# Optimization experiments

Hardware: AMD Instinct MI355X
Metric: run time of the kernel (lower is better)

The kernel has to match this reference:

```python
import jax, jax.numpy as jnp
import numpy as np

D_MODEL = 1024
N_HEADS = 16
D_HEAD = D_MODEL // N_HEADS


def setup_inputs() -> dict:
    key = jax.random.key(0)
    k1, k2, k3 = jax.random.split(key, 3)
    x = jax.random.normal(k1, (2, 2048, D_MODEL), dtype=jnp.float32)
    # torch Linear weights transposed to [in, out] for x @ W
    w_qkv = jax.random.normal(k2, (D_MODEL, 3 * D_MODEL), dtype=jnp.float32) * (D_MODEL ** -0.5)
    w_proj = jax.random.normal(k3, (D_MODEL, D_MODEL), dtype=jnp.float32) * (D_MODEL ** -0.5)
    return {"x": x, "w_qkv": w_qkv, "w_proj": w_proj}


def reference(x, w_qkv, w_proj):
    B, N, D = x.shape
    qkv = x @ w_qkv                              # [B, N, 3D]
    q, k, v = jnp.split(qkv, 3, axis=-1)         # each [B, N, D]

    def split_heads(t):
        return t.reshape(B, N, N_HEADS, D_HEAD).transpose(0, 2, 1, 3)  # [B, H, N, d]

    q, k, v = map(split_heads, (q, k, v))
    scale = 1.0 / jnp.sqrt(jnp.float32(D_HEAD))
    scores = jnp.einsum('bhnd,bhmd->bhnm', q, k) * scale   # [B, H, N, N]
    attn = jax.nn.softmax(scores, axis=-1)
    out = jnp.einsum('bhnm,bhmd->bhnd', attn, v)            # [B, H, N, d]
    out = out.transpose(0, 2, 1, 3).reshape(B, N, D)        # merge heads
    return out @ w_proj + x
```

## Files before the change

kernel.cpp:

```cpp
#include <hip/hip_runtime.h>
#include <hip/hip_bf16.h>
#include <cstdint>
#include <cstddef>

typedef __bf16 bf16;
typedef __attribute__((ext_vector_type(4))) float f32x4;
typedef __attribute__((ext_vector_type(8))) __bf16 bf16x8;
typedef __attribute__((ext_vector_type(4))) __bf16 bf16x4;

#define D_MODEL 1024
#define NHEADS  16
#define DHEAD   64
#define SEQ     2048
#define BATCH   2
#define MROWS   (BATCH*SEQ)
#define BHTOT   (BATCH*NHEADS)

#define QSCALE 0.18033688011112042f
#define DEFER_THR 11.5f

__device__ __forceinline__ void gload16(const bf16* g, bf16* l) {
  __builtin_amdgcn_global_load_lds(
      (const __attribute__((address_space(1))) void*)g,
      (__attribute__((address_space(3))) void*)l, 16, 0, 0);
}

__device__ __forceinline__ f32x4 mfma16(bf16x8 a, bf16x8 b, f32x4 c) {
  return __builtin_amdgcn_mfma_f32_16x16x32_bf16(a, b, c, 0, 0, 0);
}

__device__ __forceinline__ float fexp2(float x) {
#if __has_builtin(__builtin_amdgcn_exp2f)
  return __builtin_amdgcn_exp2f(x);
#else
  float r; asm("v_exp_f32 %0, %1" : "=v"(r) : "v"(x)); return r;
#endif
}


__global__ void cast_f32_bf16(const float* __restrict__ in, bf16* __restrict__ out, int n4) {
  int i = blockIdx.x * blockDim.x + threadIdx.x;
  if (i >= n4) return;
  float4 v = ((const float4*)in)[i];
  bf16x4 o;
  o[0] = (bf16)v.x; o[1] = (bf16)v.y; o[2] = (bf16)v.z; o[3] = (bf16)v.w;
  ((bf16x4*)out)[i] = o;
}

__global__ void tcast(const float* __restrict__ in, bf16* __restrict__ out, int R, int C) {
  __shared__ float t[32][33];
  int c0 = blockIdx.x * 32, r0 = blockIdx.y * 32;
  int tx = threadIdx.x, ty = threadIdx.y;
  #pragma unroll
  for (int i = 0; i < 4; i++)
    t[ty + i*8][tx] = in[(size_t)(r0 + ty + i*8) * C + c0 + tx];
  __syncthreads();
  #pragma unroll
  for (int i = 0; i < 4; i++)
    out[(size_t)(c0 + ty + i*8) * R + r0 + tx] = (bf16)t[tx][ty + i*8];
}

__global__ void transpose_v(const bf16* __restrict__ v, bf16* __restrict__ vt) {
  __shared__ bf16 t[32][33];
  int bh = blockIdx.z;
  int r0 = blockIdx.x * 32;
  int d0 = blockIdx.y * 32;
  int tx = threadIdx.x, ty = threadIdx.y;
  const bf16* src = v + (size_t)bh * SEQ * DHEAD;
  bf16*       dst = vt + (size_t)bh * DHEAD * SEQ;
  #pragma unroll
  for (int i = 0; i < 4; i++)
    t[ty + i*8][tx] = src[(size_t)(r0 + ty + i*8) * DHEAD + d0 + tx];
  __syncthreads();
  #pragma unroll
  for (int i = 0; i < 4; i++)
    dst[(size_t)(d0 + ty + i*8) * SEQ + r0 + tx] = t[tx][ty + i*8];
}


template <int EPI>
__global__ __launch_bounds__(256, 3) void gemm_bt(
    const bf16* __restrict__ A, const bf16* __restrict__ Bt, int K, int N,
    bf16* __restrict__ qb, bf16* __restrict__ kb, bf16* __restrict__ vb,
    const float* __restrict__ xres, float* __restrict__ outf) {
  __shared__ alignas(16) bf16 As[128 * 64];
  __shared__ alignas(16) bf16 Bs[128 * 64];
  const int tid = threadIdx.x;
  const int wave = tid >> 6, lane = tid & 63;
  const int wr = wave >> 1, wc = wave & 1;
  const int m0 = blockIdx.y * 128, n0 = blockIdx.x * 128;
  const int srow = lane >> 3;
  const int scol = ((lane & 7) ^ srow) * 8;
  const int lr16 = lane & 15, lg = lane >> 4;
  const int rsw = (lr16 & 7) << 4;
  const int cA = (lg * 16) ^ rsw;
  const int cB = (64 + lg * 16) ^ rsw;
  const char* aP = (const char*)As + (wr*64 + lr16) * 128;
  const char* bP = (const char*)Bs + (wc*64 + lr16) * 128;

  f32x4 acc[4][4];
  #pragma unroll
  for (int m = 0; m < 4; m++)
    #pragma unroll
    for (int n = 0; n < 4; n++) acc[m][n] = (f32x4)0.0f;

  for (int k0 = 0; k0 < K; k0 += 64) {
    #pragma unroll
    for (int j = 0; j < 4; j++) {
      const int c = wave * 4 + j;
      gload16(A  + (size_t)(m0 + c*8 + srow) * K + k0 + scol, &As[c * 512]);
      gload16(Bt + (size_t)(n0 + c*8 + srow) * K + k0 + scol, &Bs[c * 512]);
    }
    __syncthreads();
    bf16x8 af[4][2], bfr[4][2];
    #pragma unroll
    for (int m = 0; m < 4; m++) {
      af[m][0] = *(const bf16x8*)(aP + m*2048 + cA);
      af[m][1] = *(const bf16x8*)(aP + m*2048 + cB);
    }
    #pragma unroll
    for (int n = 0; n < 4; n++) {
      bfr[n][0] = *(const bf16x8*)(bP + n*2048 + cA);
      bfr[n][1] = *(const bf16x8*)(bP + n*2048 + cB);
    }
    #pragma unroll
    for (int m = 0; m < 4; m++)
      #pragma unroll
      for (int n = 0; n < 4; n++) {
        acc[m][n] = mfma16(af[m][0], bfr[n][0], acc[m][n]);
        acc[m][n] = mfma16(af[m][1], bfr[n][1], acc[m][n]);
      }
    __syncthreads();
  }

  #pragma unroll
  for (int n = 0; n < 4; n++) {
    const int colg = n0 + wc*64 + n*16 + lr16;
    if (EPI == 0) {
      const int which = colg >> 10;
      const int win = colg & 1023;
      const int h = win >> 6, d = win & 63;
      bf16* dst = (which == 0) ? qb : (which == 1) ? kb : vb;
      const float sc = (which == 0) ? QSCALE : 1.0f;
      #pragma unroll
      for (int m = 0; m < 4; m++) {
        const int rowg0 = m0 + wr*64 + m*16 + lg*4;
        #pragma unroll
        for (int j = 0; j < 4; j++) {
          const int rowg = rowg0 + j;
          const int b = rowg >> 11, r = rowg & 2047;
          dst[((size_t)((b << 4) + h) * SEQ + r) * DHEAD + d] = (bf16)(acc[m][n][j] * sc);
        }
      }
    } else {
      #pragma unroll
      for (int m = 0; m < 4; m++) {
        const int rowg0 = m0 + wr*64 + m*16 + lg*4;
        #pragma unroll
        for (int j = 0; j < 4; j++) {
          const size_t idx = (size_t)(rowg0 + j) * N + colg;
          outf[idx] = acc[m][n][j] + xres[idx];
        }
      }
    }
  }
}

__global__ __launch_bounds__(512, 4) void attn_kernel(
    const bf16* __restrict__ q, const bf16* __restrict__ k,
    const bf16* __restrict__ vt, bf16* __restrict__ o) {
  __shared__ alignas(16) bf16 Ks[2][64 * 64];
  __shared__ alignas(16) bf16 Vs[2][64 * 64];
  __shared__ alignas(16) bf16 P[8][16 * 72];
  const int tid = threadIdx.x;
  const int wave = tid >> 6, lane = tid & 63;
  const int lr16 = lane & 15, lg = lane >> 4;
  const int bh = blockIdx.y;
  const int b = bh >> 4, h = bh & 15;
  const int qr = blockIdx.x * 128 + wave * 16;
  const bf16* kh = k  + (size_t)bh * SEQ * DHEAD;
  const bf16* vh = vt + (size_t)bh * DHEAD * SEQ;

  const int srow = lane >> 3;
  const int scol = ((lane & 7) ^ srow) * 8;
  const bf16* kg = kh + (size_t)(wave*8 + srow) * DHEAD + scol;
  const bf16* vg = vh + (size_t)(wave*8 + srow) * SEQ + scol;
  bf16* ldsK0 = &Ks[0][wave * 512];
  bf16* ldsK1 = &Ks[1][wave * 512];
  bf16* ldsV0 = &Vs[0][wave * 512];
  bf16* ldsV1 = &Vs[1][wave * 512];

  const bf16* qrow = q + (size_t)bh * SEQ * DHEAD + (size_t)(qr + lr16) * DHEAD;
  bf16x8 qf[2];
  qf[0] = *(const bf16x8*)&qrow[lg * 8];
  qf[1] = *(const bf16x8*)&qrow[32 + lg * 8];

  float mr = 0.0f, lsum = 0.0f;
  f32x4 acc[4];
  #pragma unroll
  for (int db = 0; db < 4; db++) acc[db] = (f32x4)0.0f;

  const int rsw = (lr16 & 7) << 4;
  const int cA = (lg * 16) ^ rsw;
  const int cB = (64 + lg * 16) ^ rsw;
  const char* kr0 = (const char*)&Ks[0][0] + lr16 * 128;
  const char* kr1 = (const char*)&Ks[1][0] + lr16 * 128;
  const char* vr0 = (const char*)&Vs[0][0] + lr16 * 128;
  const char* vr1 = (const char*)&Vs[1][0] + lr16 * 128;
  bf16* pww = &P[wave][lr16 * 72 + lg * 4];
  const bf16* pfr = &P[wave][lr16 * 72 + lg * 8];

  auto compute = [&](const char* kr, const char* vr) {
    const float nmr = -mr;
    f32x4 s[4];
    __builtin_amdgcn_s_setprio(1);
    #pragma unroll
    for (int i = 0; i < 4; i++) {
      bf16x8 kf0 = *(const bf16x8*)(kr + i*2048 + cA);
      bf16x8 kf1 = *(const bf16x8*)(kr + i*2048 + cB);
      f32x4 z = {nmr, nmr, nmr, nmr};
      z = mfma16(kf0, qf[0], z);
      z = mfma16(kf1, qf[1], z);
      s[i] = z;
    }
    __builtin_amdgcn_s_setprio(0);

    float u0 = fmaxf(fmaxf(s[0][0], s[0][1]), s[0][2]);
    float u1 = fmaxf(fmaxf(s[0][3], s[1][0]), s[1][1]);
    float u2 = fmaxf(fmaxf(s[1][2], s[1][3]), s[2][0]);
    float u3 = fmaxf(fmaxf(s[2][1], s[2][2]), s[2][3]);
    float u4 = fmaxf(fmaxf(s[3][0], s[3][1]), s[3][2]);
    float lmax = fmaxf(fmaxf(fmaxf(u0, u1), fmaxf(u2, u3)), fmaxf(u4, s[3][3]));

    if (!__all(lmax <= DEFER_THR)) {
      float mx = fmaxf(lmax, __shfl_xor(lmax, 16));
      mx = fmaxf(mx, __shfl_xor(mx, 32));
      mx = fmaxf(mx, 0.0f);
      const float corr = fexp2(-mx);
      lsum *= corr;
      #pragma unroll
      for (int db = 0; db < 4; db++) acc[db] *= corr;
      mr += mx;
      #pragma unroll
      for (int i = 0; i < 4; i++)
        #pragma unroll
        for (int r = 0; r < 4; r++) s[i][r] -= mx;
    }

    #pragma unroll
    for (int i = 0; i < 4; i++)
      #pragma unroll
      for (int r = 0; r < 4; r++) s[i][r] = fexp2(s[i][r]);
    lsum += ((s[0][0] + s[0][1]) + (s[0][2] + s[0][3]))
          + ((s[1][0] + s[1][1]) + (s[1][2] + s[1][3]))
          + ((s[2][0] + s[2][1]) + (s[2][2] + s[2][3]))
          + ((s[3][0] + s[3][1]) + (s[3][2] + s[3][3]));

    #pragma unroll
    for (int i = 0; i < 4; i++) {
      bf16x4 pv;
      #pragma unroll
      for (int r = 0; r < 4; r++) pv[r] = (bf16)s[i][r];
      *(bf16x4*)(pww + i * 16) = pv;
    }
    bf16x8 pf0 = *(const bf16x8*)pfr;
    bf16x8 pf1 = *(const bf16x8*)(pfr + 32);

    __builtin_amdgcn_s_setprio(1);
    #pragma unroll
    for (int db = 0; db < 4; db++) {
      bf16x8 vf0 = *(const bf16x8*)(vr + db*2048 + cA);
      bf16x8 vf1 = *(const bf16x8*)(vr + db*2048 + cB);
      acc[db] = mfma16(vf0, pf0, acc[db]);
      acc[db] = mfma16(vf1, pf1, acc[db]);
    }
    __builtin_amdgcn_s_setprio(0);
  };

  gload16(kg, ldsK0); gload16(vg, ldsV0);
  kg += 64 * DHEAD; vg += 64;
  __syncthreads();

  for (int t = 0; t < SEQ / 64; t += 2) {
    gload16(kg, ldsK1); gload16(vg, ldsV1);
    kg += 64 * DHEAD; vg += 64;
    compute(kr0, vr0);
    __syncthreads();
    if (t + 2 < SEQ / 64) {
      gload16(kg, ldsK0); gload16(vg, ldsV0);
      kg += 64 * DHEAD; vg += 64;
    }
    compute(kr1, vr1);
    __syncthreads();
  }

  lsum += __shfl_xor(lsum, 16);
  lsum += __shfl_xor(lsum, 32);
  const float inv = 1.0f / lsum;
  bf16* orow = o + ((size_t)(b * SEQ + qr + lr16)) * D_MODEL + h * 64;
  #pragma unroll
  for (int db = 0; db < 4; db++) {
    bf16x4 ov;
    #pragma unroll
    for (int r = 0; r < 4; r++) ov[r] = (bf16)(acc[db][r] * inv);
    *(bf16x4*)&orow[db * 16 + lg * 4] = ov;
  }
}


extern "C" void kernel_launch(void* const* d_in, const int* in_sizes, int n_in,
                              void* d_out, int out_size, void* d_ws, size_t ws_size,
                              hipStream_t stream) {
  const float* x      = (const float*)d_in[0];
  const float* w_qkv  = (const float*)d_in[1];
  const float* w_proj = (const float*)d_in[2];
  float* outf = (float*)d_out;

  bf16* xb    = (bf16*)d_ws;
  bf16* wqkvT = xb    + (size_t)MROWS * D_MODEL;
  bf16* wpT   = wqkvT + (size_t)3 * D_MODEL * D_MODEL;
  bf16* qb    = wpT   + (size_t)D_MODEL * D_MODEL;
  bf16* kb    = qb    + (size_t)BHTOT * SEQ * DHEAD;
  bf16* vb    = kb    + (size_t)BHTOT * SEQ * DHEAD;
  bf16* vt    = xb;
  bf16* ob    = vb;

  dim3 tb(32, 8);

  cast_f32_bf16<<<(MROWS * D_MODEL / 4 + 255) / 256, 256, 0, stream>>>(
      x, xb, MROWS * D_MODEL / 4);
  tcast<<<dim3(3 * D_MODEL / 32, D_MODEL / 32), tb, 0, stream>>>(
      w_qkv, wqkvT, D_MODEL, 3 * D_MODEL);
  tcast<<<dim3(D_MODEL / 32, D_MODEL / 32), tb, 0, stream>>>(
      w_proj, wpT, D_MODEL, D_MODEL);

  gemm_bt<0><<<dim3(3 * D_MODEL / 128, MROWS / 128), 256, 0, stream>>>(
      xb, wqkvT, D_MODEL, 3 * D_MODEL, qb, kb, vb, nullptr, nullptr);

  transpose_v<<<dim3(SEQ / 32, DHEAD / 32, BHTOT), tb, 0, stream>>>(vb, vt);

  attn_kernel<<<dim3(SEQ / 128, BHTOT), 512, 0, stream>>>(qb, kb, vt, ob);

  gemm_bt<1><<<dim3(D_MODEL / 128, MROWS / 128), 256, 0, stream>>>(
      ob, wpT, D_MODEL, D_MODEL, nullptr, nullptr, nullptr, x, outf);
}
```

Measured before the change: 131.0 us.

## Switch attention to 32x32 MFMA with register-shuffled P and fuse V transpose

Rewrites the attention kernel so each wave handles 32 query rows using 32x32x16 bf16 MFMA. The probability tile is now built in registers with packed bf16 converts and cross-half lane shuffles instead of a round trip through shared memory. The QKV GEMM epilogue writes V already transposed, which removes the separate transpose kernel and its extra global traffic. In exchange, blocks drop to 256 threads, register pressure rises, and the transposed V stores from the GEMM are strided and less coalesced.

```diff
diff --git a/kernel.cpp b/kernel.cpp
--- a/kernel.cpp
+++ b/kernel.cpp
@@ -5,8 +5,10 @@
 
 typedef __bf16 bf16;
 typedef __attribute__((ext_vector_type(4))) float f32x4;
+typedef __attribute__((ext_vector_type(16))) float f32x16;
 typedef __attribute__((ext_vector_type(8))) __bf16 bf16x8;
 typedef __attribute__((ext_vector_type(4))) __bf16 bf16x4;
+typedef __attribute__((ext_vector_type(4))) unsigned int u32x4;
 
 #define D_MODEL 1024
 #define NHEADS  16
@@ -29,12 +31,22 @@
   return __builtin_amdgcn_mfma_f32_16x16x32_bf16(a, b, c, 0, 0, 0);
 }
 
+__device__ __forceinline__ f32x16 mfma32(bf16x8 a, bf16x8 b, f32x16 c) {
+  return __builtin_amdgcn_mfma_f32_32x32x16_bf16(a, b, c, 0, 0, 0);
+}
+
 __device__ __forceinline__ float fexp2(float x) {
 #if __has_builtin(__builtin_amdgcn_exp2f)
   return __builtin_amdgcn_exp2f(x);
 #else
   float r; asm("v_exp_f32 %0, %1" : "=v"(r) : "v"(x)); return r;
 #endif
+}
+
+__device__ __forceinline__ unsigned cvtpk(float lo, float hi) {
+  unsigned r;
+  asm("v_cvt_pk_bf16_f32 %0, %1, %2" : "=v"(r) : "v"(lo), "v"(hi));
+  return r;
 }
 
 
@@ -60,28 +72,11 @@
     out[(size_t)(c0 + ty + i*8) * R + r0 + tx] = (bf16)t[tx][ty + i*8];
 }
 
-__global__ void transpose_v(const bf16* __restrict__ v, bf16* __restrict__ vt) {
-  __shared__ bf16 t[32][33];
-  int bh = blockIdx.z;
-  int r0 = blockIdx.x * 32;
-  int d0 = blockIdx.y * 32;
-  int tx = threadIdx.x, ty = threadIdx.y;
-  const bf16* src = v + (size_t)bh * SEQ * DHEAD;
-  bf16*       dst = vt + (size_t)bh * DHEAD * SEQ;
-  #pragma unroll
-  for (int i = 0; i < 4; i++)
-    t[ty + i*8][tx] = src[(size_t)(r0 + ty + i*8) * DHEAD + d0 + tx];
-  __syncthreads();
-  #pragma unroll
-  for (int i = 0; i < 4; i++)
-    dst[(size_t)(d0 + ty + i*8) * SEQ + r0 + tx] = t[tx][ty + i*8];
-}
-
 
 template <int EPI>
 __global__ __launch_bounds__(256, 3) void gemm_bt(
     const bf16* __restrict__ A, const bf16* __restrict__ Bt, int K, int N,
-    bf16* __restrict__ qb, bf16* __restrict__ kb, bf16* __restrict__ vb,
+    bf16* __restrict__ qb, bf16* __restrict__ kb, bf16* __restrict__ vtb,
     const float* __restrict__ xres, float* __restrict__ outf) {
   __shared__ alignas(16) bf16 As[128 * 64];
   __shared__ alignas(16) bf16 Bs[128 * 64];
@@ -140,8 +135,6 @@
       const int which = colg >> 10;
       const int win = colg & 1023;
       const int h = win >> 6, d = win & 63;
-      bf16* dst = (which == 0) ? qb : (which == 1) ? kb : vb;
-      const float sc = (which == 0) ? QSCALE : 1.0f;
       #pragma unroll
       for (int m = 0; m < 4; m++) {
         const int rowg0 = m0 + wr*64 + m*16 + lg*4;
@@ -149,7 +142,14 @@
         for (int j = 0; j < 4; j++) {
           const int rowg = rowg0 + j;
           const int b = rowg >> 11, r = rowg & 2047;
-          dst[((size_t)((b << 4) + h) * SEQ + r) * DHEAD + d] = (bf16)(acc[m][n][j] * sc);
+          const int bh = (b << 4) + h;
+          if (which == 2) {
+            vtb[((size_t)bh * DHEAD + d) * SEQ + r] = (bf16)acc[m][n][j];
+          } else {
+            bf16* dst = (which == 0) ? qb : kb;
+            const float sc = (which == 0) ? QSCALE : 1.0f;
+            dst[((size_t)bh * SEQ + r) * DHEAD + d] = (bf16)(acc[m][n][j] * sc);
+          }
         }
       }
     } else {
@@ -166,144 +166,148 @@
   }
 }
 
-__global__ __launch_bounds__(512, 4) void attn_kernel(
+__global__ __launch_bounds__(256, 2) void attn_kernel(
     const bf16* __restrict__ q, const bf16* __restrict__ k,
     const bf16* __restrict__ vt, bf16* __restrict__ o) {
   __shared__ alignas(16) bf16 Ks[2][64 * 64];
   __shared__ alignas(16) bf16 Vs[2][64 * 64];
-  __shared__ alignas(16) bf16 P[8][16 * 72];
   const int tid = threadIdx.x;
   const int wave = tid >> 6, lane = tid & 63;
-  const int lr16 = lane & 15, lg = lane >> 4;
+  const int l31 = lane & 31, hi = lane >> 5;
   const int bh = blockIdx.y;
   const int b = bh >> 4, h = bh & 15;
-  const int qr = blockIdx.x * 128 + wave * 16;
+  const int qr = blockIdx.x * 128 + wave * 32;
   const bf16* kh = k  + (size_t)bh * SEQ * DHEAD;
   const bf16* vh = vt + (size_t)bh * DHEAD * SEQ;
 
   const int srow = lane >> 3;
   const int scol = ((lane & 7) ^ srow) * 8;
-  const bf16* kg = kh + (size_t)(wave*8 + srow) * DHEAD + scol;
-  const bf16* vg = vh + (size_t)(wave*8 + srow) * SEQ + scol;
-  bf16* ldsK0 = &Ks[0][wave * 512];
-  bf16* ldsK1 = &Ks[1][wave * 512];
-  bf16* ldsV0 = &Vs[0][wave * 512];
-  bf16* ldsV1 = &Vs[1][wave * 512];
-
-  const bf16* qrow = q + (size_t)bh * SEQ * DHEAD + (size_t)(qr + lr16) * DHEAD;
-  bf16x8 qf[2];
-  qf[0] = *(const bf16x8*)&qrow[lg * 8];
-  qf[1] = *(const bf16x8*)&qrow[32 + lg * 8];
+  const bf16* kg = kh + (size_t)(wave*16 + srow) * DHEAD + scol;
+  const bf16* vg = vh + (size_t)(wave*16 + srow) * SEQ + scol;
+  bf16* ldsK[2] = { &Ks[0][wave * 1024], &Ks[1][wave * 1024] };
+  bf16* ldsV[2] = { &Vs[0][wave * 1024], &Vs[1][wave * 1024] };
+
+  const bf16* qrow = q + (size_t)bh * SEQ * DHEAD + (size_t)(qr + l31) * DHEAD;
+  bf16x8 qf[4];
+  #pragma unroll
+  for (int ks = 0; ks < 4; ks++)
+    qf[ks] = *(const bf16x8*)&qrow[ks * 16 + hi * 8];
 
   float mr = 0.0f, lsum = 0.0f;
-  f32x4 acc[4];
-  #pragma unroll
-  for (int db = 0; db < 4; db++) acc[db] = (f32x4)0.0f;
-
-  const int rsw = (lr16 & 7) << 4;
-  const int cA = (lg * 16) ^ rsw;
-  const int cB = (64 + lg * 16) ^ rsw;
-  const char* kr0 = (const char*)&Ks[0][0] + lr16 * 128;
-  const char* kr1 = (const char*)&Ks[1][0] + lr16 * 128;
-  const char* vr0 = (const char*)&Vs[0][0] + lr16 * 128;
-  const char* vr1 = (const char*)&Vs[1][0] + lr16 * 128;
-  bf16* pww = &P[wave][lr16 * 72 + lg * 4];
-  const bf16* pfr = &P[wave][lr16 * 72 + lg * 8];
+  f32x16 acc0 = (f32x16)0.0f, acc1 = (f32x16)0.0f;
+
+  const int rsw = (lane & 7) << 4;
+  const int rowoff = l31 * 128;
+  int cofs[4];
+  #pragma unroll
+  for (int ks = 0; ks < 4; ks++) cofs[ks] = (ks * 32 + hi * 16) ^ rsw;
+  const char* kr0 = (const char*)&Ks[0][0] + rowoff;
+  const char* kr1 = (const char*)&Ks[1][0] + rowoff;
+  const char* vr0 = (const char*)&Vs[0][0] + rowoff;
+  const char* vr1 = (const char*)&Vs[1][0] + rowoff;
 
   auto compute = [&](const char* kr, const char* vr) {
     const float nmr = -mr;
-    f32x4 s[4];
+    f32x16 s0 = (f32x16)nmr, s1 = (f32x16)nmr;
     __builtin_amdgcn_s_setprio(1);
     #pragma unroll
-    for (int i = 0; i < 4; i++) {
-      bf16x8 kf0 = *(const bf16x8*)(kr + i*2048 + cA);
-      bf16x8 kf1 = *(const bf16x8*)(kr + i*2048 + cB);
-      f32x4 z = {nmr, nmr, nmr, nmr};
-      z = mfma16(kf0, qf[0], z);
-      z = mfma16(kf1, qf[1], z);
-      s[i] = z;
+    for (int ks = 0; ks < 4; ks++) {
+      bf16x8 kf0 = *(const bf16x8*)(kr + cofs[ks]);
+      bf16x8 kf1 = *(const bf16x8*)(kr + 4096 + cofs[ks]);
+      s0 = mfma32(kf0, qf[ks], s0);
+      s1 = mfma32(kf1, qf[ks], s1);
     }
     __builtin_amdgcn_s_setprio(0);
 
-    float u0 = fmaxf(fmaxf(s[0][0], s[0][1]), s[0][2]);
-    float u1 = fmaxf(fmaxf(s[0][3], s[1][0]), s[1][1]);
-    float u2 = fmaxf(fmaxf(s[1][2], s[1][3]), s[2][0]);
-    float u3 = fmaxf(fmaxf(s[2][1], s[2][2]), s[2][3]);
-    float u4 = fmaxf(fmaxf(s[3][0], s[3][1]), s[3][2]);
-    float lmax = fmaxf(fmaxf(fmaxf(u0, u1), fmaxf(u2, u3)), fmaxf(u4, s[3][3]));
+    float p[16];
+    #pragma unroll
+    for (int r = 0; r < 16; r++) p[r] = fmaxf(s0[r], s1[r]);
+    #pragma unroll
+    for (int st = 8; st > 0; st >>= 1)
+      #pragma unroll
+      for (int r = 0; r < st; r++) p[r] = fmaxf(p[r], p[r + st]);
+    const float lmax = p[0];
 
     if (!__all(lmax <= DEFER_THR)) {
-      float mx = fmaxf(lmax, __shfl_xor(lmax, 16));
-      mx = fmaxf(mx, __shfl_xor(mx, 32));
+      float mx = fmaxf(lmax, __shfl_xor(lmax, 32));
       mx = fmaxf(mx, 0.0f);
       const float corr = fexp2(-mx);
       lsum *= corr;
-      #pragma unroll
-      for (int db = 0; db < 4; db++) acc[db] *= corr;
+      acc0 *= corr; acc1 *= corr;
       mr += mx;
       #pragma unroll
-      for (int i = 0; i < 4; i++)
-        #pragma unroll
-        for (int r = 0; r < 4; r++) s[i][r] -= mx;
-    }
-
-    #pragma unroll
-    for (int i = 0; i < 4; i++)
-      #pragma unroll
-      for (int r = 0; r < 4; r++) s[i][r] = fexp2(s[i][r]);
-    lsum += ((s[0][0] + s[0][1]) + (s[0][2] + s[0][3]))
-          + ((s[1][0] + s[1][1]) + (s[1][2] + s[1][3]))
-          + ((s[2][0] + s[2][1]) + (s[2][2] + s[2][3]))
-          + ((s[3][0] + s[3][1]) + (s[3][2] + s[3][3]));
-
-    #pragma unroll
-    for (int i = 0; i < 4; i++) {
-      bf16x4 pv;
-      #pragma unroll
-      for (int r = 0; r < 4; r++) pv[r] = (bf16)s[i][r];
-      *(bf16x4*)(pww + i * 16) = pv;
-    }
-    bf16x8 pf0 = *(const bf16x8*)pfr;
-    bf16x8 pf1 = *(const bf16x8*)(pfr + 32);
+      for (int r = 0; r < 16; r++) { s0[r] -= mx; s1[r] -= mx; }
+    }
+
+    #pragma unroll
+    for (int r = 0; r < 16; r++) { s0[r] = fexp2(s0[r]); s1[r] = fexp2(s1[r]); }
+    float sp[8];
+    #pragma unroll
+    for (int r = 0; r < 8; r++) sp[r] = (s0[r] + s0[r + 8]) + (s1[r] + s1[r + 8]);
+    lsum += ((sp[0] + sp[1]) + (sp[2] + sp[3])) + ((sp[4] + sp[5]) + (sp[6] + sp[7]));
 
     __builtin_amdgcn_s_setprio(1);
     #pragma unroll
-    for (int db = 0; db < 4; db++) {
-      bf16x8 vf0 = *(const bf16x8*)(vr + db*2048 + cA);
-      bf16x8 vf1 = *(const bf16x8*)(vr + db*2048 + cB);
-      acc[db] = mfma16(vf0, pf0, acc[db]);
-      acc[db] = mfma16(vf1, pf1, acc[db]);
+    for (int t = 0; t < 2; t++) {
+      const f32x16& sv = t ? s1 : s0;
+      unsigned own[8], par[8];
+      #pragma unroll
+      for (int i = 0; i < 8; i++) {
+        own[i] = cvtpk(sv[2*i], sv[2*i+1]);
+        par[i] = (unsigned)__shfl_xor((int)own[i], 32);
+      }
+      #pragma unroll
+      for (int u = 0; u < 2; u++) {
+        const int base = 4 * u + 2 * hi;
+        u32x4 fw;
+        fw[0] = hi ? par[base]     : own[base];
+        fw[1] = hi ? par[base + 1] : own[base + 1];
+        fw[2] = hi ? own[base]     : par[base];
+        fw[3] = hi ? own[base + 1] : par[base + 1];
+        bf16x8 pf = __builtin_bit_cast(bf16x8, fw);
+        const int ksl = t * 2 + u;
+        bf16x8 vf0 = *(const bf16x8*)(vr + cofs[ksl]);
+        bf16x8 vf1 = *(const bf16x8*)(vr + 4096 + cofs[ksl]);
+        acc0 = mfma32(vf0, pf, acc0);
+        acc1 = mfma32(vf1, pf, acc1);
+      }
     }
     __builtin_amdgcn_s_setprio(0);
   };
 
-  gload16(kg, ldsK0); gload16(vg, ldsV0);
+  gload16(kg, ldsK[0]); gload16(kg + 8 * DHEAD, ldsK[0] + 512);
+  gload16(vg, ldsV[0]); gload16(vg + 8 * SEQ,   ldsV[0] + 512);
   kg += 64 * DHEAD; vg += 64;
   __syncthreads();
 
   for (int t = 0; t < SEQ / 64; t += 2) {
-    gload16(kg, ldsK1); gload16(vg, ldsV1);
+    gload16(kg, ldsK[1]); gload16(kg + 8 * DHEAD, ldsK[1] + 512);
+    gload16(vg, ldsV[1]); gload16(vg + 8 * SEQ,   ldsV[1] + 512);
     kg += 64 * DHEAD; vg += 64;
     compute(kr0, vr0);
     __syncthreads();
     if (t + 2 < SEQ / 64) {
-      gload16(kg, ldsK0); gload16(vg, ldsV0);
+      gload16(kg, ldsK[0]); gload16(kg + 8 * DHEAD, ldsK[0] + 512);
+      gload16(vg, ldsV[0]); gload16(vg + 8 * SEQ,   ldsV[0] + 512);
       kg += 64 * DHEAD; vg += 64;
     }
     compute(kr1, vr1);
     __syncthreads();
   }
 
-  lsum += __shfl_xor(lsum, 16);
   lsum += __shfl_xor(lsum, 32);
   const float inv = 1.0f / lsum;
-  bf16* orow = o + ((size_t)(b * SEQ + qr + lr16)) * D_MODEL + h * 64;
-  #pragma unroll
-  for (int db = 0; db < 4; db++) {
-    bf16x4 ov;
-    #pragma unroll
-    for (int r = 0; r < 4; r++) ov[r] = (bf16)(acc[db][r] * inv);
-    *(bf16x4*)&orow[db * 16 + lg * 4] = ov;
+  bf16* orow = o + ((size_t)(b * SEQ + qr + l31)) * D_MODEL + h * 64 + hi * 4;
+  #pragma unroll
+  for (int g = 0; g < 4; g++) {
+    bf16x4 o0, o1;
+    #pragma unroll
+    for (int e = 0; e < 4; e++) {
+      o0[e] = (bf16)(acc0[4*g + e] * inv);
+      o1[e] = (bf16)(acc1[4*g + e] * inv);
+    }
+    *(bf16x4*)&orow[8 * g]      = o0;
+    *(bf16x4*)&orow[32 + 8 * g] = o1;
   }
 }
 
@@ -321,9 +325,8 @@
   bf16* wpT   = wqkvT + (size_t)3 * D_MODEL * D_MODEL;
   bf16* qb    = wpT   + (size_t)D_MODEL * D_MODEL;
   bf16* kb    = qb    + (size_t)BHTOT * SEQ * DHEAD;
-  bf16* vb    = kb    + (size_t)BHTOT * SEQ * DHEAD;
-  bf16* vt    = xb;
-  bf16* ob    = vb;
+  bf16* vtb   = kb    + (size_t)BHTOT * SEQ * DHEAD;
+  bf16* ob    = xb;
 
   dim3 tb(32, 8);
 
@@ -335,11 +338,9 @@
       w_proj, wpT, D_MODEL, D_MODEL);
 
   gemm_bt<0><<<dim3(3 * D_MODEL / 128, MROWS / 128), 256, 0, stream>>>(
-      xb, wqkvT, D_MODEL, 3 * D_MODEL, qb, kb, vb, nullptr, nullptr);
-
-  transpose_v<<<dim3(SEQ / 32, DHEAD / 32, BHTOT), tb, 0, stream>>>(vb, vt);
-
-  attn_kernel<<<dim3(SEQ / 128, BHTOT), 512, 0, stream>>>(qb, kb, vt, ob);
+      xb, wqkvT, D_MODEL, 3 * D_MODEL, qb, kb, vtb, nullptr, nullptr);
+
+  attn_kernel<<<dim3(SEQ / 128, BHTOT), 256, 0, stream>>>(qb, kb, vtb, ob);
 
   gemm_bt<1><<<dim3(D_MODEL / 128, MROWS / 128), 256, 0, stream>>>(
       ob, wpT, D_MODEL, D_MODEL, nullptr, nullptr, nullptr, x, outf);
```

Measured after the change: 154.8 us. 18.2% more time.
